# Optimization experiments

Measured on AMD Instinct MI355X. Metric: run time of the kernel, lower is better.

Reference implementation:

```python
import jax, jax.numpy as jnp
import numpy as np

TEMPERATURE = 0.07
BN_EPS = 1e-5
NORM_EPS = 1e-12


def _forward_features(x, conv_w, conv_b, gamma, beta, lin_w, lin_b):
    # prepend_relu
    x = jax.nn.relu(x)
    # 1x1 conv: [B, Cin, H, W] x [Cout, Cin] -> [B, Cout, H, W]
    x = jnp.einsum('bihw,oi->bohw', x, conv_w) + conv_b[None, :, None, None]
    # BatchNorm2d, training mode (biased batch stats over N,H,W per channel)
    mu = x.mean(axis=(0, 2, 3))
    var = x.var(axis=(0, 2, 3))
    x = (x - mu[None, :, None, None]) * jax.lax.rsqrt(var + BN_EPS)[None, :, None, None]
    x = x * gamma[None, :, None, None] + beta[None, :, None, None]
    x = jax.nn.relu(x)
    # second 1x1 conv ('linear')
    x = jnp.einsum('bihw,oi->bohw', x, lin_w) + lin_b[None, :, None, None]
    # append_normalize: F.normalize(p=2, dim=1)
    norm = jnp.sqrt(jnp.sum(x * x, axis=1, keepdims=True))
    x = x / jnp.maximum(norm, NORM_EPS)
    return x


def _dense_info_nce(o, t):
    # o, t: [B, C, H, W]
    B, C, H, W = t.shape
    o = o.transpose(0, 2, 3, 1).reshape(B, H * W, C)  # [B, HW, C]
    t = t.transpose(0, 2, 3, 1).reshape(B, H * W, C)
    pos = jnp.einsum('bik,bik->bi', o, t) / TEMPERATURE          # [B, HW]
    logits = jnp.einsum('bik,bjk->bij', o, t) / TEMPERATURE      # [B, HW, HW]
    lse = jax.nn.logsumexp(logits, axis=-1)                      # [B, HW]
    return jnp.mean(lse - pos)


def setup_inputs() -> dict:
    key = jax.random.key(0)
    ks = jax.random.split(key, 4)
    B, Cin, Cout, H, W = 8, 256, 128, 60, 60
    x_orig = jax.random.normal(ks[0], (B, Cin, H, W), jnp.float32)
    x_trans = jax.random.normal(ks[1], (B, Cin, H, W), jnp.float32)
    conv_w = jax.random.normal(ks[2], (Cout, Cin), jnp.float32) * (1.0 / np.sqrt(Cin))
    conv_b = jnp.zeros((Cout,), jnp.float32)
    gamma = jnp.ones((Cout,), jnp.float32)
    beta = jnp.zeros((Cout,), jnp.float32)
    lin_w = jax.random.normal(ks[3], (Cout, Cout), jnp.float32) * (1.0 / np.sqrt(Cout))
    lin_b = jnp.zeros((Cout,), jnp.float32)
    return {"x_orig": x_orig, "x_trans": x_trans, "conv_w": conv_w, "conv_b": conv_b,
            "gamma": gamma, "beta": beta, "lin_w": lin_w, "lin_b": lin_b}


def reference(x_orig, x_trans, conv_w, conv_b, gamma, beta, lin_w, lin_b):
    o = _forward_features(x_orig, conv_w, conv_b, gamma, beta, lin_w, lin_b)
    t = _forward_features(x_trans, conv_w, conv_b, gamma, beta, lin_w, lin_b)
    return _dense_info_nce(o, t)
```

## Files before the change

### kernel.cpp

```cpp
#include <hip/hip_runtime.h>
#include <hip/hip_bf16.h>

#define HW 3600
#define NQ 28800
#define CIN 256
#define CMID 128

typedef short bf16x8 __attribute__((ext_vector_type(8)));
typedef float f32x4 __attribute__((ext_vector_type(4)));

#define INV_T 14.285714285714286f
#define SQRT_INV_T 3.7796447300922722f
#define LOG2E 1.4426950408889634f
#define NM (-20.60992915555662f)

__device__ inline unsigned short f2bf(float f) {
  unsigned u = __float_as_uint(f);
  return (unsigned short)((u + 0x7fffu + ((u >> 16) & 1u)) >> 16);
}
__device__ inline float bf2f(unsigned short h) { return __uint_as_float((unsigned)h << 16); }

__global__ void prep_kernel(const float* __restrict__ conv_w, const float* __restrict__ lin_w,
                            unsigned short* __restrict__ cw16, unsigned short* __restrict__ lw16) {
  const int i = blockIdx.x * 256 + threadIdx.x;
  if (i < 128 * 256) cw16[i] = f2bf(conv_w[i]);
  if (i < 128 * 128) lw16[i] = f2bf(lin_w[i]);
}

__global__ __launch_bounds__(256, 4) void conv1_mfma_kernel(
    const float* __restrict__ x0, const float* __restrict__ x1,
    const unsigned short* __restrict__ cw16,
    unsigned short* __restrict__ yt, float* __restrict__ stats) {
  __shared__ __align__(16) unsigned short xT[64 * 32];
  __shared__ float sredw[4][128];
  __shared__ float s2redw[4][128];
  const int z = blockIdx.z;
  const float* x = z ? x1 : x0;
  float* st = stats + z * 256;
  unsigned short* yz = yt + (size_t)z * NQ * 128;

  const int t = threadIdx.x;
  const int w = t >> 6;
  const int l = t & 63;
  const int lr = l & 15;
  const int lg = l >> 4;
  const int q0 = blockIdx.x * 64;

  f32x4 acc[8];
#pragma unroll
  for (int tile = 0; tile < 8; tile++) acc[tile] = (f32x4){0.f, 0.f, 0.f, 0.f};

  const int qcol = q0 + 4 * (t & 15);
  const int bb = qcol / HW;
  const int pp = qcol - bb * HW;
  const float* xcol = x + (size_t)bb * CIN * HW + pp;
  const int cil0 = (t >> 4);
  const int cil1 = cil0 + 16;

  float4 v0 = *(const float4*)&xcol[(size_t)cil0 * HW];
  float4 v1 = *(const float4*)&xcol[(size_t)cil1 * HW];

  for (int ch = 0; ch < 8; ch++) {
    if (ch) __syncthreads();
    {
      unsigned short* dst = &xT[(4 * (t & 15)) * 32 + cil0];
      dst[0]  = f2bf(fmaxf(v0.x, 0.f));
      dst[32] = f2bf(fmaxf(v0.y, 0.f));
      dst[64] = f2bf(fmaxf(v0.z, 0.f));
      dst[96] = f2bf(fmaxf(v0.w, 0.f));
      dst = &xT[(4 * (t & 15)) * 32 + cil1];
      dst[0]  = f2bf(fmaxf(v1.x, 0.f));
      dst[32] = f2bf(fmaxf(v1.y, 0.f));
      dst[64] = f2bf(fmaxf(v1.z, 0.f));
      dst[96] = f2bf(fmaxf(v1.w, 0.f));
    }
    __syncthreads();
    if (ch < 7) {
      v0 = *(const float4*)&xcol[(size_t)((ch + 1) * 32 + cil0) * HW];
      v1 = *(const float4*)&xcol[(size_t)((ch + 1) * 32 + cil1) * HW];
    }
    bf16x8 bv = *(const bf16x8*)&xT[(w * 16 + lr) * 32 + lg * 8];
#pragma unroll
    for (int tile = 0; tile < 8; tile++) {
      bf16x8 av = *(const bf16x8*)&cw16[(size_t)(tile * 16 + lr) * 256 + ch * 32 + lg * 8];
      acc[tile] = __builtin_amdgcn_mfma_f32_16x16x32_bf16(av, bv, acc[tile], 0, 0, 0);
    }
  }

#pragma unroll
  for (int tile = 0; tile < 8; tile++) {
#pragma unroll
    for (int i = 0; i < 4; i++) {
      float v = acc[tile][i];
      float v2 = v * v;
      v += __shfl_xor(v, 1); v2 += __shfl_xor(v2, 1);
      v += __shfl_xor(v, 2); v2 += __shfl_xor(v2, 2);
      v += __shfl_xor(v, 4); v2 += __shfl_xor(v2, 4);
      v += __shfl_xor(v, 8); v2 += __shfl_xor(v2, 8);
      if (lr == 0) {
        sredw[w][tile * 16 + lg * 4 + i] = v;
        s2redw[w][tile * 16 + lg * 4 + i] = v2;
      }
    }
  }

  const int q = q0 + w * 16 + lr;
#pragma unroll
  for (int tile = 0; tile < 8; tile++) {
    union { unsigned short u[4]; uint2 v; } pk;
#pragma unroll
    for (int i = 0; i < 4; i++) pk.u[i] = f2bf(acc[tile][i]);
    *(uint2*)&yz[(size_t)q * 128 + tile * 16 + lg * 4] = pk.v;
  }

  __syncthreads();
  if (t < 128) {
    atomicAdd(&st[t], sredw[0][t] + sredw[1][t] + sredw[2][t] + sredw[3][t]);
    atomicAdd(&st[128 + t], s2redw[0][t] + s2redw[1][t] + s2redw[2][t] + s2redw[3][t]);
  }
}

__global__ void scale_kernel(const float* __restrict__ stats, const float* __restrict__ conv_b,
                             const float* __restrict__ gamma, const float* __restrict__ beta,
                             float* __restrict__ sc) {
  const int z = blockIdx.x;
  const float* st = stats + z * 256;
  float* scz = sc + z * 256;
  const int c = threadIdx.x;
  const float inv_n = 1.f / (float)NQ;
  const float macc = st[c] * inv_n;
  const float var = st[128 + c] * inv_n - macc * macc;
  const float mean = macc + conv_b[c];
  const float s = gamma[c] * rsqrtf(var + 1e-5f);
  const float tt = beta[c] - mean * s;
  scz[c] = s;
  scz[128 + c] = conv_b[c] * s + tt;
}

__global__ __launch_bounds__(256, 4) void conv2_mfma_kernel(
    const unsigned short* __restrict__ yt, const unsigned short* __restrict__ lw16,
    const float* __restrict__ sc, const float* __restrict__ lin_b,
    unsigned short* __restrict__ feat_o, unsigned short* __restrict__ feat_t) {
  const int z = blockIdx.z;
  const unsigned short* yz = yt + (size_t)z * NQ * 128;
  const float* scz = sc + z * 256;
  unsigned short* feat = z ? feat_t : feat_o;

  const int t = threadIdx.x;
  const int w = t >> 6;
  const int l = t & 63;
  const int lr = l & 15;
  const int lg = l >> 4;
  const int q = blockIdx.x * 64 + w * 16 + lr;

  f32x4 acc[8];
#pragma unroll
  for (int tile = 0; tile < 8; tile++) acc[tile] = (f32x4){0.f, 0.f, 0.f, 0.f};

  const unsigned short* yrow = yz + (size_t)q * 128;
  for (int ch = 0; ch < 4; ch++) {
    bf16x8 raw = *(const bf16x8*)&yrow[ch * 32 + lg * 8];
    bf16x8 bv;
#pragma unroll
    for (int e = 0; e < 8; e++) {
      const int c = ch * 32 + lg * 8 + e;
      float v = fmaxf(fmaf(bf2f((unsigned short)raw[e]), scz[c], scz[128 + c]), 0.f);
      bv[e] = (short)f2bf(v);
    }
#pragma unroll
    for (int tile = 0; tile < 8; tile++) {
      bf16x8 av = *(const bf16x8*)&lw16[(size_t)(tile * 16 + lr) * 128 + ch * 32 + lg * 8];
      acc[tile] = __builtin_amdgcn_mfma_f32_16x16x32_bf16(av, bv, acc[tile], 0, 0, 0);
    }
  }

  float vals[8][4];
  float ssq = 0.f;
#pragma unroll
  for (int tile = 0; tile < 8; tile++) {
#pragma unroll
    for (int i = 0; i < 4; i++) {
      float v = acc[tile][i] + lin_b[tile * 16 + lg * 4 + i];
      vals[tile][i] = v;
      ssq += v * v;
    }
  }
  ssq += __shfl_xor(ssq, 16);
  ssq += __shfl_xor(ssq, 32);
  const float inv = SQRT_INV_T / fmaxf(sqrtf(ssq), 1e-12f);

#pragma unroll
  for (int tile = 0; tile < 8; tile++) {
    union { unsigned short u[4]; uint2 v; } pk;
#pragma unroll
    for (int i = 0; i < 4; i++) pk.u[i] = f2bf(vals[tile][i] * inv);
    *(uint2*)&feat[(size_t)q * 128 + tile * 16 + lg * 4] = pk.v;
  }
}

__global__ __launch_bounds__(256, 2) void infonce_kernel(
    const unsigned short* __restrict__ fo, const unsigned short* __restrict__ ft,
    float* __restrict__ sumexp) {
  const int b = blockIdx.z;
  const int t = threadIdx.x;
  const int w = t >> 6;
  const int lane = t & 63;
  const int lr = lane & 15;
  const int lkq = lane >> 4;
  const int base = blockIdx.x * 256 + w * 64;
  if (base >= HW) return;
  const unsigned short* fob = fo + (size_t)b * HW * 128;
  const unsigned short* ftb = ft + (size_t)b * HW * 128;

  bf16x8 a[4][4];
#pragma unroll
  for (int tile = 0; tile < 4; tile++) {
    const int r = min(base + tile * 16 + lr, HW - 1);
    const unsigned short* ap = fob + (size_t)r * 128 + lkq * 8;
#pragma unroll
    for (int kk = 0; kk < 4; kk++) a[tile][kk] = *(const bf16x8*)(ap + kk * 32);
  }
  float rs[4][4];
#pragma unroll
  for (int tile = 0; tile < 4; tile++)
#pragma unroll
    for (int i = 0; i < 4; i++) rs[tile][i] = 0.f;

  for (int ch = blockIdx.y; ch < 75; ch += 15) {
    const int cbase = ch * 48;
    bf16x8 bv[3][4];
#pragma unroll
    for (int sub = 0; sub < 3; sub++) {
      const unsigned short* bp = ftb + (size_t)(cbase + sub * 16 + lr) * 128 + lkq * 8;
#pragma unroll
      for (int kk = 0; kk < 4; kk++) bv[sub][kk] = *(const bf16x8*)(bp + kk * 32);
    }
    f32x4 acc[4][3];
#pragma unroll
    for (int tile = 0; tile < 4; tile++)
#pragma unroll
      for (int sub = 0; sub < 3; sub++) acc[tile][sub] = (f32x4){0.f, 0.f, 0.f, 0.f};
#pragma unroll
    for (int kk = 0; kk < 4; kk++)
#pragma unroll
      for (int tile = 0; tile < 4; tile++)
#pragma unroll
        for (int sub = 0; sub < 3; sub++)
          acc[tile][sub] = __builtin_amdgcn_mfma_f32_16x16x32_bf16(
              a[tile][kk], bv[sub][kk], acc[tile][sub], 0, 0, 0);
#pragma unroll
    for (int tile = 0; tile < 4; tile++)
#pragma unroll
      for (int sub = 0; sub < 3; sub++)
#pragma unroll
        for (int i = 0; i < 4; i++)
          rs[tile][i] += exp2f(fmaf(acc[tile][sub][i], LOG2E, NM));
  }
#pragma unroll
  for (int tile = 0; tile < 4; tile++)
#pragma unroll
    for (int i = 0; i < 4; i++) {
      float v = rs[tile][i];
      v += __shfl_xor(v, 1); v += __shfl_xor(v, 2);
      v += __shfl_xor(v, 4); v += __shfl_xor(v, 8);
      rs[tile][i] = v;
    }
  if (lr == 0) {
#pragma unroll
    for (int tile = 0; tile < 4; tile++)
#pragma unroll
      for (int i = 0; i < 4; i++) {
        const int r = base + tile * 16 + lkq * 4 + i;
        if (r < HW) atomicAdd(&sumexp[b * HW + r], rs[tile][i]);
      }
  }
}

__global__ __launch_bounds__(256) void final_kernel(
    const float* __restrict__ sumexp, const unsigned short* __restrict__ fo,
    const unsigned short* __restrict__ ft, float* __restrict__ out) {
  const int q = blockIdx.x * 256 + threadIdx.x;
  float val = 0.f;
  if (q < NQ) {
    const unsigned short* a = fo + (size_t)q * 128;
    const unsigned short* c = ft + (size_t)q * 128;
    float dot = 0.f;
#pragma unroll
    for (int k = 0; k < 128; k += 8) {
      bf16x8 ua = *(const bf16x8*)(a + k);
      bf16x8 ub = *(const bf16x8*)(c + k);
#pragma unroll
      for (int e = 0; e < 8; e++)
        dot = fmaf(bf2f((unsigned short)ua[e]), bf2f((unsigned short)ub[e]), dot);
    }
    val = logf(sumexp[q]) + INV_T - dot;
  }
#pragma unroll
  for (int m = 1; m < 64; m <<= 1) val += __shfl_xor(val, m);
  __shared__ float red[4];
  const int wid = threadIdx.x >> 6;
  if ((threadIdx.x & 63) == 0) red[wid] = val;
  __syncthreads();
  if (threadIdx.x == 0)
    atomicAdd(out, (red[0] + red[1] + red[2] + red[3]) * (1.f / (float)NQ));
}

extern "C" void kernel_launch(void* const* d_in, const int* in_sizes, int n_in,
                              void* d_out, int out_size, void* d_ws, size_t ws_size,
                              hipStream_t stream) {
  (void)in_sizes; (void)n_in; (void)out_size; (void)ws_size;
  const float* x_orig = (const float*)d_in[0];
  const float* x_trans = (const float*)d_in[1];
  const float* conv_w = (const float*)d_in[2];
  const float* conv_b = (const float*)d_in[3];
  const float* gamma = (const float*)d_in[4];
  const float* beta = (const float*)d_in[5];
  const float* lin_w = (const float*)d_in[6];
  const float* lin_b = (const float*)d_in[7];
  float* out = (float*)d_out;

  char* ws = (char*)d_ws;
  unsigned short* yt = (unsigned short*)(ws + 0);
  unsigned short* cw16 = (unsigned short*)(ws + 14745600);
  unsigned short* lw16 = (unsigned short*)(ws + 14811136);
  float* stats = (float*)(ws + 14843904);
  float* sc = (float*)(ws + 14845952);
  float* sumexp = (float*)(ws + 14848000);
  unsigned short* feat_o = (unsigned short*)(ws + 14963200);
  unsigned short* feat_t = (unsigned short*)(ws + 22336000);

  hipMemsetAsync(ws + 14843904, 0, 2048 + 2048 + 115200, stream);
  hipMemsetAsync(d_out, 0, sizeof(float), stream);

  prep_kernel<<<128, 256, 0, stream>>>(conv_w, lin_w, cw16, lw16);

  conv1_mfma_kernel<<<dim3(450, 1, 2), 256, 0, stream>>>(x_orig, x_trans, cw16, yt, stats);
  scale_kernel<<<2, 128, 0, stream>>>(stats, conv_b, gamma, beta, sc);
  conv2_mfma_kernel<<<dim3(450, 1, 2), 256, 0, stream>>>(yt, lw16, sc, lin_b, feat_o, feat_t);

  infonce_kernel<<<dim3(15, 15, 8), 256, 0, stream>>>(feat_o, feat_t, sumexp);
  final_kernel<<<113, 256, 0, stream>>>(sumexp, feat_o, feat_t, out);
}
```

Measured before the change: 258.9 us.

## Stage InfoNCE key tiles in double-buffered LDS and shard BN stat atomics

The InfoNCE kernel now has the four waves of a block share each 48-row key tile through a double-buffered shared-memory buffer. The next tile is prefetched into registers while MFMAs run on the current one, and each block walks a contiguous range of 15 column chunks over a flattened 600-block grid. This removes the fourfold redundant per-wave global loads of key features. The cost is a barrier per iteration, and waves past the end of the last row block now stay alive to take part in the barrier. Separately, conv1 batch-norm statistics are spread over 16 shards to cut same-address atomic contention, with scale_kernel summing the shards.

New measurement: 250.1 us. 3.4% less time.

```diff
diff --git a/kernel.cpp b/kernel.cpp
--- a/kernel.cpp
+++ b/kernel.cpp
@@ -5,6 +5,7 @@
 #define NQ 28800
 #define CIN 256
 #define CMID 128
+#define NSHARD 16
 
 typedef short bf16x8 __attribute__((ext_vector_type(8)));
 typedef float f32x4 __attribute__((ext_vector_type(4)));
@@ -36,7 +37,7 @@
   __shared__ float s2redw[4][128];
   const int z = blockIdx.z;
   const float* x = z ? x1 : x0;
-  float* st = stats + z * 256;
+  float* st = stats + (z * NSHARD + (blockIdx.x & (NSHARD - 1))) * 256;
   unsigned short* yz = yt + (size_t)z * NQ * 128;
 
   const int t = threadIdx.x;
@@ -124,12 +125,18 @@
                              const float* __restrict__ gamma, const float* __restrict__ beta,
                              float* __restrict__ sc) {
   const int z = blockIdx.x;
-  const float* st = stats + z * 256;
+  const float* st = stats + z * NSHARD * 256;
   float* scz = sc + z * 256;
   const int c = threadIdx.x;
+  float s1 = 0.f, s2 = 0.f;
+#pragma unroll
+  for (int sh = 0; sh < NSHARD; sh++) {
+    s1 += st[sh * 256 + c];
+    s2 += st[sh * 256 + 128 + c];
+  }
   const float inv_n = 1.f / (float)NQ;
-  const float macc = st[c] * inv_n;
-  const float var = st[128 + c] * inv_n - macc * macc;
+  const float macc = s1 * inv_n;
+  const float var = s2 * inv_n - macc * macc;
   const float mean = macc + conv_b[c];
   const float s = gamma[c] * rsqrtf(var + 1e-5f);
   const float tt = beta[c] - mean * s;
@@ -194,21 +201,25 @@
     union { unsigned short u[4]; uint2 v; } pk;
 #pragma unroll
     for (int i = 0; i < 4; i++) pk.u[i] = f2bf(vals[tile][i] * inv);
-    *(uint2*)&feat[(size_t)q * 128 + tile * 16 + lg * 4] = pk.v;
+    *(uint2*)&feat[(size_t)q * 128 + tile * 16 + tile * 0 + lg * 4] = pk.v;
   }
 }
 
 __global__ __launch_bounds__(256, 2) void infonce_kernel(
     const unsigned short* __restrict__ fo, const unsigned short* __restrict__ ft,
     float* __restrict__ sumexp) {
-  const int b = blockIdx.z;
+  __shared__ __align__(16) unsigned short Bs[2][6144];
+  const int id = blockIdx.x;
+  const int b = id & 7;
+  const int within = id >> 3;
+  const int rowblk = within % 15;
+  const int colg = within / 15;
   const int t = threadIdx.x;
   const int w = t >> 6;
   const int lane = t & 63;
   const int lr = lane & 15;
   const int lkq = lane >> 4;
-  const int base = blockIdx.x * 256 + w * 64;
-  if (base >= HW) return;
+  const int base = rowblk * 256 + w * 64;
   const unsigned short* fob = fo + (size_t)b * HW * 128;
   const unsigned short* ftb = ft + (size_t)b * HW * 128;
 
@@ -226,14 +237,32 @@
 #pragma unroll
     for (int i = 0; i < 4; i++) rs[tile][i] = 0.f;
 
-  for (int ch = blockIdx.y; ch < 75; ch += 15) {
-    const int cbase = ch * 48;
-    bf16x8 bv[3][4];
-#pragma unroll
-    for (int sub = 0; sub < 3; sub++) {
-      const unsigned short* bp = ftb + (size_t)(cbase + sub * 16 + lr) * 128 + lkq * 8;
-#pragma unroll
-      for (int kk = 0; kk < 4; kk++) bv[sub][kk] = *(const bf16x8*)(bp + kk * 32);
+  int rowoff[3];
+#pragma unroll
+  for (int i = 0; i < 3; i++) {
+    const int f = i * 4 + w;
+    const int kk = f / 3;
+    const int sub = f - kk * 3;
+    rowoff[i] = (sub * 16 + lr) * 128 + kk * 32 + lkq * 8;
+  }
+
+  uint4 r[3];
+  {
+    const unsigned short* p = ftb + (size_t)(colg * 15) * 48 * 128;
+#pragma unroll
+    for (int i = 0; i < 3; i++) r[i] = *(const uint4*)(p + rowoff[i]);
+  }
+
+  for (int it = 0; it < 15; it++) {
+    unsigned short* bufp = &Bs[it & 1][0];
+#pragma unroll
+    for (int i = 0; i < 3; i++)
+      *(uint4*)&bufp[(i * 4 + w) * 512 + lane * 8] = r[i];
+    __syncthreads();
+    if (it < 14) {
+      const unsigned short* p = ftb + (size_t)((colg * 15 + it + 1)) * 48 * 128;
+#pragma unroll
+      for (int i = 0; i < 3; i++) r[i] = *(const uint4*)(p + rowoff[i]);
     }
     f32x4 acc[4][3];
 #pragma unroll
@@ -241,13 +270,18 @@
 #pragma unroll
       for (int sub = 0; sub < 3; sub++) acc[tile][sub] = (f32x4){0.f, 0.f, 0.f, 0.f};
 #pragma unroll
-    for (int kk = 0; kk < 4; kk++)
+    for (int kk = 0; kk < 4; kk++) {
+      bf16x8 bv[3];
+#pragma unroll
+      for (int sub = 0; sub < 3; sub++)
+        bv[sub] = *(const bf16x8*)&bufp[(kk * 3 + sub) * 512 + lane * 8];
 #pragma unroll
       for (int tile = 0; tile < 4; tile++)
 #pragma unroll
         for (int sub = 0; sub < 3; sub++)
           acc[tile][sub] = __builtin_amdgcn_mfma_f32_16x16x32_bf16(
-              a[tile][kk], bv[sub][kk], acc[tile][sub], 0, 0, 0);
+              a[tile][kk], bv[sub], acc[tile][sub], 0, 0, 0);
+    }
 #pragma unroll
     for (int tile = 0; tile < 4; tile++)
 #pragma unroll
@@ -256,6 +290,7 @@
         for (int i = 0; i < 4; i++)
           rs[tile][i] += exp2f(fmaf(acc[tile][sub][i], LOG2E, NM));
   }
+
 #pragma unroll
   for (int tile = 0; tile < 4; tile++)
 #pragma unroll
@@ -270,8 +305,8 @@
     for (int tile = 0; tile < 4; tile++)
 #pragma unroll
       for (int i = 0; i < 4; i++) {
-        const int r = base + tile * 16 + lkq * 4 + i;
-        if (r < HW) atomicAdd(&sumexp[b * HW + r], rs[tile][i]);
+        const int rr = base + tile * 16 + lkq * 4 + i;
+        if (rr < HW) atomicAdd(&sumexp[b * HW + rr], rs[tile][i]);
       }
   }
 }
@@ -324,12 +359,12 @@
   unsigned short* cw16 = (unsigned short*)(ws + 14745600);
   unsigned short* lw16 = (unsigned short*)(ws + 14811136);
   float* stats = (float*)(ws + 14843904);
-  float* sc = (float*)(ws + 14845952);
-  float* sumexp = (float*)(ws + 14848000);
-  unsigned short* feat_o = (unsigned short*)(ws + 14963200);
-  unsigned short* feat_t = (unsigned short*)(ws + 22336000);
-
-  hipMemsetAsync(ws + 14843904, 0, 2048 + 2048 + 115200, stream);
+  float* sc = (float*)(ws + 14876672);
+  float* sumexp = (float*)(ws + 14878720);
+  unsigned short* feat_o = (unsigned short*)(ws + 14993920);
+  unsigned short* feat_t = (unsigned short*)(ws + 22366720);
+
+  hipMemsetAsync(ws + 14843904, 0, 32768 + 2048 + 115200, stream);
   hipMemsetAsync(d_out, 0, sizeof(float), stream);
 
   prep_kernel<<<128, 256, 0, stream>>>(conv_w, lin_w, cw16, lw16);
@@ -338,6 +373,6 @@
   scale_kernel<<<2, 128, 0, stream>>>(stats, conv_b, gamma, beta, sc);
   conv2_mfma_kernel<<<dim3(450, 1, 2), 256, 0, stream>>>(yt, lw16, sc, lin_b, feat_o, feat_t);
 
-  infonce_kernel<<<dim3(15, 15, 8), 256, 0, stream>>>(feat_o, feat_t, sumexp);
+  infonce_kernel<<<600, 256, 0, stream>>>(feat_o, feat_t, sumexp);
   final_kernel<<<113, 256, 0, stream>>>(sumexp, feat_o, feat_t, out);
 }
```
